# Optimization experiments

Measured on AMD Instinct MI355X. Metric: run time of the kernel, lower is better.

## Reference

```python
import jax, jax.numpy as jnp
import numpy as np

B, N, F, H = 8, 256, 512, 256  # batch, nodes (=hidden_dim), feature_dim, hidden_dim


def _pair_scores(x, y, W1a, W1b, b1, W2, b2):
    """sigmoid(MLP(concat(x_i, y_j))) for all pairs, without materializing concat.

    x, y: [B, N, H]. W1a/W1b are the two halves of the Linear(2H -> H) weight.
    Returns [B, N, N].
    """
    a = jnp.einsum('bnh,hk->bnk', x, W1a)          # contribution of row i
    c = jnp.einsum('bnh,hk->bnk', y, W1b)          # contribution of row j
    h = jax.nn.relu(a[:, :, None, :] + c[:, None, :, :] + b1)  # [B,N,N,H]
    s = jnp.einsum('bijh,h->bij', h, W2) + b2
    return jax.nn.sigmoid(s)


def setup_inputs() -> dict:
    key = jax.random.key(0)
    ks = jax.random.split(key, 16)
    sc = 0.02
    return {
        'image_features': jax.random.normal(ks[0], (B, N, F), jnp.float32),
        'text_features': jax.random.normal(ks[1], (B, N, F), jnp.float32),
        # feature_transform: Linear(F->H), ReLU, Linear(H->H)
        'ft_W1': jax.random.normal(ks[2], (F, H), jnp.float32) * sc,
        'ft_b1': jnp.zeros((H,), jnp.float32),
        'ft_W2': jax.random.normal(ks[3], (H, H), jnp.float32) * sc,
        'ft_b2': jnp.zeros((H,), jnp.float32),
        # structure_learning: Linear(2H->H) split into two H x H halves, Linear(H->1)
        'sl_W1a': jax.random.normal(ks[4], (H, H), jnp.float32) * sc,
        'sl_W1b': jax.random.normal(ks[5], (H, H), jnp.float32) * sc,
        'sl_b1': jnp.zeros((H,), jnp.float32),
        'sl_W2': jax.random.normal(ks[6], (H,), jnp.float32) * sc,
        'sl_b2': jnp.zeros((), jnp.float32),
        # causal_net: Linear(2H->H) split, Linear(H->1)
        'cn_W1a': jax.random.normal(ks[7], (H, H), jnp.float32) * sc,
        'cn_W1b': jax.random.normal(ks[8], (H, H), jnp.float32) * sc,
        'cn_b1': jnp.zeros((H,), jnp.float32),
        'cn_W2': jax.random.normal(ks[9], (H,), jnp.float32) * sc,
        'cn_b2': jnp.zeros((), jnp.float32),
    }


def reference(image_features, text_features,
              ft_W1, ft_b1, ft_W2, ft_b2,
              sl_W1a, sl_W1b, sl_b1, sl_W2, sl_b2,
              cn_W1a, cn_W1b, cn_b1, cn_W2, cn_b2):
    # --- StructuralLearning ---
    def feat(x):
        h = jax.nn.relu(jnp.einsum('bnf,fh->bnh', x, ft_W1) + ft_b1)
        return jnp.einsum('bnh,hk->bnk', h, ft_W2) + ft_b2

    img_h = feat(image_features)   # [B,N,H]
    txt_h = feat(text_features)    # [B,N,H]
    structure = _pair_scores(img_h, txt_h, sl_W1a, sl_W1b, sl_b1, sl_W2, sl_b2)  # [B,N,N]

    # --- CausalDiscovery (batched over all node pairs; sigmoid(structure) > 0
    # everywhere so every (i,j) is an edge). DAG cycle removal is a CPU-side
    # networkx post-process and is omitted from the differentiable reference. ---
    causal_matrix = _pair_scores(structure, structure, cn_W1a, cn_W1b, cn_b1, cn_W2, cn_b2)

    # --- verify_causal_invariance ---
    stability = jnp.mean(jnp.abs(causal_matrix - jnp.roll(causal_matrix, 1, axis=0)))
    consistency = jnp.mean(jnp.std(causal_matrix, axis=0, ddof=1))  # torch.std is unbiased
    invariance_score = 1.0 - (stability + consistency) / 2

    return structure, causal_matrix, invariance_score
```

## Files before the change

### kernel.cpp

```cpp
#include <hip/hip_runtime.h>
#include <math.h>

#define B_ 8
#define N_ 256
#define F_ 512
#define H_ 256

typedef __attribute__((ext_vector_type(8))) short short8;
typedef __attribute__((ext_vector_type(4))) float floatx4;

__device__ __forceinline__ unsigned int f2bf_bits(float f) {
    unsigned int u = __float_as_uint(f);
    return (u + 0x7fffu + ((u >> 16) & 1u)) >> 16;
}
__device__ __forceinline__ unsigned int pack2bf(float a, float b) {
    return f2bf_bits(a) | (f2bf_bits(b) << 16);
}

__global__ __launch_bounds__(256) void prep_weights(
    const float* __restrict__ ftW1, const float* __restrict__ ftW2,
    const float* __restrict__ slW1a, const float* __restrict__ slW1b,
    const float* __restrict__ cnW1a, const float* __restrict__ cnW1b,
    const float* __restrict__ ftb2, const float* __restrict__ slb1,
    unsigned short* __restrict__ wt, float* __restrict__ bA, float* __restrict__ bB)
{
    if (blockIdx.x >= 224) {
        const int second = (blockIdx.x == 225);
        const float* W = second ? slW1b : slW1a;
        const int n = threadIdx.x;
        float s0 = 0.f, s1 = 0.f, s2 = 0.f, s3 = 0.f;
#pragma unroll 4
        for (int k = 0; k < 256; k += 4) {
            s0 = fmaf(ftb2[k],     W[(k)     * 256 + n], s0);
            s1 = fmaf(ftb2[k + 1], W[(k + 1) * 256 + n], s1);
            s2 = fmaf(ftb2[k + 2], W[(k + 2) * 256 + n], s2);
            s3 = fmaf(ftb2[k + 3], W[(k + 3) * 256 + n], s3);
        }
        float s = (s0 + s1) + (s2 + s3);
        if (second) bB[n] = s + slb1[n];
        else        bA[n] = s;
        return;
    }

    int t = blockIdx.x * 256 + threadIdx.x;
    if (t < 49152) {
        const float* src; int K; unsigned short* dst;
        if (t < 16384) { src = ftW1; K = 512; dst = wt; }
        else {
            int m  = (t - 16384) >> 13;
            t = (t - 16384) & 8191; K = 256;
            switch (m) {
                case 0:  src = slW1a; dst = wt + 131072; break;
                case 1:  src = slW1b; dst = wt + 196608; break;
                case 2:  src = cnW1a; dst = wt + 262144; break;
                default: src = cnW1b; dst = wt + 327680; break;
            }
        }
        const int n  = t & 255;
        const int k0 = (t >> 8) * 8;
        unsigned int p[4];
#pragma unroll
        for (int j = 0; j < 4; ++j) {
            float f0 = src[(size_t)(k0 + 2 * j)     * 256 + n];
            float f1 = src[(size_t)(k0 + 2 * j + 1) * 256 + n];
            p[j] = pack2bf(f0, f1);
        }
        *(uint4*)(dst + (size_t)n * K + k0) = make_uint4(p[0], p[1], p[2], p[3]);
    } else {
        const int lt = t - 49152;
        const int k  = lt >> 5;
        const int n0 = (lt & 31) * 8;
        const float* src = ftW2 + (size_t)k * 256 + n0;
        float4 f0 = *(const float4*)(src);
        float4 f1 = *(const float4*)(src + 4);
        unsigned short* dst = wt + 393216 + (size_t)k * 256 + n0;
        *(uint4*)dst = make_uint4(pack2bf(f0.x, f0.y), pack2bf(f0.z, f0.w),
                                  pack2bf(f1.x, f1.y), pack2bf(f1.z, f1.w));
    }
}

__global__ __launch_bounds__(256) void gemm_mfma(
    const void* __restrict__ A0, const void* __restrict__ A1, int aSplitBlk, int aBf16,
    const unsigned short* __restrict__ Wt0, const unsigned short* __restrict__ Wt1,
    const float* __restrict__ bias0, const float* __restrict__ bias1,
    int wRowSplitBlk, int wColSplitBlk,
    void* __restrict__ out, int outBf16, int ldOut, int K, int relu)
{
    __shared__ unsigned short As[2][64][40];
    __shared__ unsigned short Bs[2][64][40];

    const int tid = threadIdx.x;
    const int bx = blockIdx.x, by = blockIdx.y;

    const void* Abase; int arow0;
    if (by < aSplitBlk) { Abase = A0; arow0 = by * 64; }
    else                { Abase = A1; arow0 = (by - aSplitBlk) * 64; }

    int wcolBlk = bx;
    bool second;
    if (wColSplitBlk > 0) {
        second = (bx >= wColSplitBlk);
        if (second) wcolBlk = bx - wColSplitBlk;
    } else {
        second = (by >= wRowSplitBlk);
    }
    const unsigned short* Wt = second ? Wt1 : Wt0;
    const float* bias        = second ? bias1 : bias0;
    const int wcol = wcolBlk * 64;

    const int r    = tid >> 2;
    const int kq   = (tid & 3) * 8;
    const int lane = tid & 63;
    const int wv   = tid >> 6;
    const int col  = lane & 15;
    const int quad = lane >> 4;

    floatx4 acc[4] = {};

    uint4 apack, bpack;
    float4 af0, af1;
    const unsigned short* Abf = (const unsigned short*)Abase + (size_t)(arow0 + r) * K + kq;
    const float*          Afp = (const float*)Abase + (size_t)(arow0 + r) * K + kq;
    const unsigned short* Wp  = Wt + (size_t)(wcol + r) * K + kq;

    if (aBf16) apack = *(const uint4*)(Abf);
    else { af0 = *(const float4*)(Afp); af1 = *(const float4*)(Afp + 4); }
    bpack = *(const uint4*)(Wp);

    int p = 0;
    for (int k0 = 0; k0 < K; k0 += 32) {
        uint4 aw;
        if (aBf16) aw = apack;
        else aw = make_uint4(pack2bf(af0.x, af0.y), pack2bf(af0.z, af0.w),
                             pack2bf(af1.x, af1.y), pack2bf(af1.z, af1.w));
        uint4 bw = bpack;

        *(uint4*)&As[p][r][kq] = aw;
        *(uint4*)&Bs[p][r][kq] = bw;

        if (k0 + 32 < K) {
            if (aBf16) apack = *(const uint4*)(Abf + k0 + 32);
            else {
                af0 = *(const float4*)(Afp + k0 + 32);
                af1 = *(const float4*)(Afp + k0 + 32 + 4);
            }
            bpack = *(const uint4*)(Wp + k0 + 32);
        }

        __syncthreads();

        short8 bfrag = *(const short8*)&Bs[p][wv * 16 + col][quad * 8];
#pragma unroll
        for (int tm = 0; tm < 4; ++tm) {
            short8 afrag = *(const short8*)&As[p][tm * 16 + col][quad * 8];
            acc[tm] = __builtin_amdgcn_mfma_f32_16x16x32_bf16(afrag, bfrag, acc[tm], 0, 0, 0);
        }
        p ^= 1;
    }

    const int ocol = bx * 64 + wv * 16 + col;
    const int bcol = wcol + wv * 16 + col;
    const float bv = bias ? bias[bcol] : 0.f;
#pragma unroll
    for (int tm = 0; tm < 4; ++tm) {
#pragma unroll
        for (int rr = 0; rr < 4; ++rr) {
            float v = acc[tm][rr] + bv;
            if (relu) v = fmaxf(v, 0.f);
            const size_t o = (size_t)(by * 64 + tm * 16 + quad * 4 + rr) * ldOut + ocol;
            if (outBf16) ((unsigned short*)out)[o] = (unsigned short)f2bf_bits(v);
            else         ((float*)out)[o] = v;
        }
    }
}

__global__ __launch_bounds__(256) void pair_score(
    const float* __restrict__ Abase, int ldA,
    const float* __restrict__ Cbase, int ldC,
    const float* __restrict__ W2, const float* __restrict__ b2p,
    float* __restrict__ out)
{
    __shared__ float aS[32][256];
    __shared__ float cS[32][256];

    const int tid = threadIdx.x;
    const int b   = blockIdx.z;
    const int i0b = blockIdx.y * 32;
    const int j0b = blockIdx.x * 32;

    {
        const int r   = tid >> 3;
        const int c8  = tid & 7;
        const int key = (r >> 1) & 7;
        const float* Ar = Abase + ((size_t)b * N_ + i0b + r) * ldA;
        const float* Cr = Cbase + ((size_t)b * N_ + j0b + r) * ldC;
#pragma unroll
        for (int rep = 0; rep < 8; ++rep) {
            const int ch = c8 + rep * 8;
            float4 va = *(const float4*)(Ar + ch * 4);
            float4 vc = *(const float4*)(Cr + ch * 4);
            const int pc = (ch ^ key) << 2;
            *(float4*)&aS[r][pc] = va;
            *(float4*)&cS[r][pc] = vc;
        }
    }
    __syncthreads();

    const int ti = tid >> 4, tj = tid & 15;
    const int ia = ti * 2, jc = tj * 2;
    const int keyA = ti & 7, keyC = tj & 7;

    float s00 = 0.f, s01 = 0.f, s10 = 0.f, s11 = 0.f;
#pragma unroll 4
    for (int h = 0; h < H_; h += 4) {
        const int chunk = h >> 2;
        const int pa = (chunk ^ keyA) << 2;
        const int pc = (chunk ^ keyC) << 2;
        float4 a0 = *(const float4*)&aS[ia][pa];
        float4 a1 = *(const float4*)&aS[ia + 1][pa];
        float4 c0 = *(const float4*)&cS[jc][pc];
        float4 c1 = *(const float4*)&cS[jc + 1][pc];
        float4 w  = *(const float4*)&W2[h];
        float av0[4] = { a0.x, a0.y, a0.z, a0.w };
        float av1[4] = { a1.x, a1.y, a1.z, a1.w };
        float cv0[4] = { c0.x, c0.y, c0.z, c0.w };
        float cv1[4] = { c1.x, c1.y, c1.z, c1.w };
        float wv[4]  = { w.x,  w.y,  w.z,  w.w  };
#pragma unroll
        for (int q = 0; q < 4; ++q) {
            s00 = fmaf(fmaxf(av0[q] + cv0[q], 0.f), wv[q], s00);
            s01 = fmaf(fmaxf(av0[q] + cv1[q], 0.f), wv[q], s01);
            s10 = fmaf(fmaxf(av1[q] + cv0[q], 0.f), wv[q], s10);
            s11 = fmaf(fmaxf(av1[q] + cv1[q], 0.f), wv[q], s11);
        }
    }
    const float bb = b2p[0];
    const size_t ob = ((size_t)b * N_ + i0b + ia) * N_ + j0b + jc;
    out[ob]           = 1.f / (1.f + expf(-(s00 + bb)));
    out[ob + 1]       = 1.f / (1.f + expf(-(s01 + bb)));
    out[ob + N_]      = 1.f / (1.f + expf(-(s10 + bb)));
    out[ob + N_ + 1]  = 1.f / (1.f + expf(-(s11 + bb)));
}

__global__ __launch_bounds__(256) void invariance_partial(
    const float* __restrict__ causal, float* __restrict__ accum,
    float* __restrict__ out_scalar)
{
    const int idx = blockIdx.x * 256 + threadIdx.x;
    float x[B_];
#pragma unroll
    for (int b = 0; b < B_; ++b) x[b] = causal[(size_t)b * (N_ * N_) + idx];

    float stab = 0.f, mean = 0.f;
#pragma unroll
    for (int b = 0; b < B_; ++b) {
        stab += fabsf(x[b] - x[(b + B_ - 1) % B_]);
        mean += x[b];
    }
    mean *= (1.f / B_);
    float var = 0.f;
#pragma unroll
    for (int b = 0; b < B_; ++b) {
        float d = x[b] - mean;
        var = fmaf(d, d, var);
    }
    float sd = sqrtf(var * (1.f / (B_ - 1)));

#pragma unroll
    for (int off = 32; off > 0; off >>= 1) {
        stab += __shfl_down(stab, off, 64);
        sd   += __shfl_down(sd, off, 64);
    }

    __shared__ float red[8];
    if ((threadIdx.x & 63) == 0) {
        red[threadIdx.x >> 6]     = stab;
        red[4 + (threadIdx.x >> 6)] = sd;
    }
    __syncthreads();
    if (threadIdx.x == 0) {
        float s = (red[0] + red[1]) + (red[2] + red[3]);
        float d = (red[4] + red[5]) + (red[6] + red[7]);
        atomicAdd(&accum[0], s);
        atomicAdd(&accum[1], d);
        __threadfence();
        unsigned int prev = atomicAdd((unsigned int*)&accum[2], 1u);
        if (prev == 255u) {
            float st  = atomicAdd(&accum[0], 0.f);
            float sdt = atomicAdd(&accum[1], 0.f);
            float stability   = st  * (1.f / (float)(B_ * N_ * N_));
            float consistency = sdt * (1.f / (float)(N_ * N_));
            out_scalar[0] = 1.f - (stability + consistency) * 0.5f;
        }
    }
}

extern "C" void kernel_launch(void* const* d_in, const int* in_sizes, int n_in,
                              void* d_out, int out_size, void* d_ws, size_t ws_size,
                              hipStream_t stream)
{
    const float* img   = (const float*)d_in[0];
    const float* txt   = (const float*)d_in[1];
    const float* ftW1  = (const float*)d_in[2];
    const float* ftb1  = (const float*)d_in[3];
    const float* ftW2  = (const float*)d_in[4];
    const float* ftb2  = (const float*)d_in[5];
    const float* slW1a = (const float*)d_in[6];
    const float* slW1b = (const float*)d_in[7];
    const float* slb1  = (const float*)d_in[8];
    const float* slW2  = (const float*)d_in[9];
    const float* slb2  = (const float*)d_in[10];
    const float* cnW1a = (const float*)d_in[11];
    const float* cnW1b = (const float*)d_in[12];
    const float* cnb1  = (const float*)d_in[13];
    const float* cnW2  = (const float*)d_in[14];
    const float* cnb2  = (const float*)d_in[15];

    float* out       = (float*)d_out;
    float* structure = out;
    float* causal    = out + (size_t)B_ * N_ * N_;
    float* inv       = out + 2 * (size_t)B_ * N_ * N_;

    unsigned short* wt     = (unsigned short*)d_ws;
    unsigned short* wcombT = wt + 458752;
    float* bA    = (float*)(wt + 589824);
    float* bB    = bA + 256;
    float* accum = bA + 512;
    unsigned short* h1b = wt + 655360;
    float* acb   = (float*)(wt + 1703936);
    float* ac2b  = acb;

    hipMemsetAsync(accum, 0, 4 * sizeof(float), stream);

    dim3 blk(256);
    const int BIG = 1 << 20;

    const unsigned short* wtFT1 = wt;
    const unsigned short* wtSLA = wt + 131072;
    const unsigned short* wtSLB = wt + 196608;
    const unsigned short* wtCNA = wt + 262144;
    const unsigned short* wtCNB = wt + 327680;
    const unsigned short* ftW2r = wt + 393216;

    prep_weights<<<dim3(226), blk, 0, stream>>>(
        ftW1, ftW2, slW1a, slW1b, cnW1a, cnW1b, ftb2, slb1, wt, bA, bB);

    gemm_mfma<<<dim3(4, 8), blk, 0, stream>>>(
        wtSLA, wtSLB, 4, 1, ftW2r, ftW2r, nullptr, nullptr, BIG, 0,
        wcombT, 1, 256, 256, 0);

    gemm_mfma<<<dim3(4, 64), blk, 0, stream>>>(
        img, txt, 32, 0, wtFT1, wtFT1, ftb1, ftb1, BIG, 0,
        h1b, 1, 256, 512, 1);

    gemm_mfma<<<dim3(4, 64), blk, 0, stream>>>(
        h1b, h1b, BIG, 1, wcombT, wcombT + 65536, bA, bB, 32, 0,
        acb, 0, 256, 256, 0);

    pair_score<<<dim3(8, 8, 8), blk, 0, stream>>>(
        acb, 256, acb + (size_t)2048 * 256, 256, slW2, slb2, structure);

    gemm_mfma<<<dim3(8, 32), blk, 0, stream>>>(
        structure, structure, BIG, 0, wtCNA, wtCNB, nullptr, cnb1, BIG, 4,
        ac2b, 0, 512, 256, 0);

    pair_score<<<dim3(8, 8, 8), blk, 0, stream>>>(
        ac2b, 512, ac2b + 256, 512, cnW2, cnb2, causal);

    invariance_partial<<<dim3(N_ * N_ / 256), blk, 0, stream>>>(causal, accum, inv);
}
```

Measured before the change: 176.9 us.

## Use packed fp16 pair-score math, larger tiles, and merge two GEMM launches

The pair-score intermediates are now written by the GEMMs as fp16 instead of fp32. The pair-score kernel does the add and ReLU with packed half2 arithmetic and accumulates in fp32. Its tile grows to 64x32 with 4x2 outputs per thread, which halves LDS footprint per row and raises reuse. The first feature GEMM and the weight-combining GEMM are merged into one launch through a job struct, saving a launch and letting them overlap. The cost is reduced precision in the pre-ReLU sums, which adds accuracy risk.

```diff
diff --git a/kernel.cpp b/kernel.cpp
--- a/kernel.cpp
+++ b/kernel.cpp
@@ -8,6 +8,7 @@
 
 typedef __attribute__((ext_vector_type(8))) short short8;
 typedef __attribute__((ext_vector_type(4))) float floatx4;
+typedef _Float16 h2 __attribute__((ext_vector_type(2)));
 
 __device__ __forceinline__ unsigned int f2bf_bits(float f) {
     unsigned int u = __float_as_uint(f);
@@ -15,6 +16,19 @@
 }
 __device__ __forceinline__ unsigned int pack2bf(float a, float b) {
     return f2bf_bits(a) | (f2bf_bits(b) << 16);
+}
+__device__ __forceinline__ h2 as_h2(unsigned int u) {
+    union { unsigned int u; h2 h; } x; x.u = u; return x.h;
+}
+__device__ __forceinline__ h2 relu2(h2 t) {
+    h2 z; z.x = (_Float16)0; z.y = (_Float16)0;
+#if __has_builtin(__builtin_elementwise_max)
+    return __builtin_elementwise_max(t, z);
+#else
+    t.x = t.x > z.x ? t.x : z.x;
+    t.y = t.y > z.y ? t.y : z.y;
+    return t;
+#endif
 }
 
 __global__ __launch_bounds__(256) void prep_weights(
@@ -79,33 +93,40 @@
     }
 }
 
-__global__ __launch_bounds__(256) void gemm_mfma(
-    const void* __restrict__ A0, const void* __restrict__ A1, int aSplitBlk, int aBf16,
-    const unsigned short* __restrict__ Wt0, const unsigned short* __restrict__ Wt1,
-    const float* __restrict__ bias0, const float* __restrict__ bias1,
-    int wRowSplitBlk, int wColSplitBlk,
-    void* __restrict__ out, int outBf16, int ldOut, int K, int relu)
+struct GJob {
+    const void* A0; const void* A1; int aSplitBlk; int aBf16;
+    const unsigned short* Wt0; const unsigned short* Wt1;
+    const float* bias0; const float* bias1;
+    int wRowSplitBlk; int wColSplitBlk;
+    void* out; int outMode; int ldOut; int K; int relu;
+};
+
+__global__ __launch_bounds__(256) void gemm_mfma(GJob j0, GJob j1, int j0By)
 {
     __shared__ unsigned short As[2][64][40];
     __shared__ unsigned short Bs[2][64][40];
 
+    const bool firstJob = ((int)blockIdx.y < j0By);
+    const GJob j = firstJob ? j0 : j1;
+    const int by = firstJob ? blockIdx.y : blockIdx.y - j0By;
+    const int bx = blockIdx.x;
     const int tid = threadIdx.x;
-    const int bx = blockIdx.x, by = blockIdx.y;
+    const int K = j.K;
 
     const void* Abase; int arow0;
-    if (by < aSplitBlk) { Abase = A0; arow0 = by * 64; }
-    else                { Abase = A1; arow0 = (by - aSplitBlk) * 64; }
+    if (by < j.aSplitBlk) { Abase = j.A0; arow0 = by * 64; }
+    else                  { Abase = j.A1; arow0 = (by - j.aSplitBlk) * 64; }
 
     int wcolBlk = bx;
     bool second;
-    if (wColSplitBlk > 0) {
-        second = (bx >= wColSplitBlk);
-        if (second) wcolBlk = bx - wColSplitBlk;
+    if (j.wColSplitBlk > 0) {
+        second = (bx >= j.wColSplitBlk);
+        if (second) wcolBlk = bx - j.wColSplitBlk;
     } else {
-        second = (by >= wRowSplitBlk);
-    }
-    const unsigned short* Wt = second ? Wt1 : Wt0;
-    const float* bias        = second ? bias1 : bias0;
+        second = (by >= j.wRowSplitBlk);
+    }
+    const unsigned short* Wt = second ? j.Wt1 : j.Wt0;
+    const float* bias        = second ? j.bias1 : j.bias0;
     const int wcol = wcolBlk * 64;
 
     const int r    = tid >> 2;
@@ -123,14 +144,14 @@
     const float*          Afp = (const float*)Abase + (size_t)(arow0 + r) * K + kq;
     const unsigned short* Wp  = Wt + (size_t)(wcol + r) * K + kq;
 
-    if (aBf16) apack = *(const uint4*)(Abf);
+    if (j.aBf16) apack = *(const uint4*)(Abf);
     else { af0 = *(const float4*)(Afp); af1 = *(const float4*)(Afp + 4); }
     bpack = *(const uint4*)(Wp);
 
     int p = 0;
     for (int k0 = 0; k0 < K; k0 += 32) {
         uint4 aw;
-        if (aBf16) aw = apack;
+        if (j.aBf16) aw = apack;
         else aw = make_uint4(pack2bf(af0.x, af0.y), pack2bf(af0.z, af0.w),
                              pack2bf(af1.x, af1.y), pack2bf(af1.z, af1.w));
         uint4 bw = bpack;
@@ -139,7 +160,7 @@
         *(uint4*)&Bs[p][r][kq] = bw;
 
         if (k0 + 32 < K) {
-            if (aBf16) apack = *(const uint4*)(Abf + k0 + 32);
+            if (j.aBf16) apack = *(const uint4*)(Abf + k0 + 32);
             else {
                 af0 = *(const float4*)(Afp + k0 + 32);
                 af1 = *(const float4*)(Afp + k0 + 32 + 4);
@@ -166,80 +187,100 @@
 #pragma unroll
         for (int rr = 0; rr < 4; ++rr) {
             float v = acc[tm][rr] + bv;
-            if (relu) v = fmaxf(v, 0.f);
-            const size_t o = (size_t)(by * 64 + tm * 16 + quad * 4 + rr) * ldOut + ocol;
-            if (outBf16) ((unsigned short*)out)[o] = (unsigned short)f2bf_bits(v);
-            else         ((float*)out)[o] = v;
+            if (j.relu) v = fmaxf(v, 0.f);
+            const size_t o = (size_t)(by * 64 + tm * 16 + quad * 4 + rr) * j.ldOut + ocol;
+            if (j.outMode == 0)      ((float*)j.out)[o] = v;
+            else if (j.outMode == 1) ((unsigned short*)j.out)[o] = (unsigned short)f2bf_bits(v);
+            else                     ((_Float16*)j.out)[o] = (_Float16)v;
         }
     }
 }
 
 __global__ __launch_bounds__(256) void pair_score(
-    const float* __restrict__ Abase, int ldA,
-    const float* __restrict__ Cbase, int ldC,
+    const unsigned short* __restrict__ Abase, int ldA,
+    const unsigned short* __restrict__ Cbase, int ldC,
     const float* __restrict__ W2, const float* __restrict__ b2p,
     float* __restrict__ out)
 {
-    __shared__ float aS[32][256];
-    __shared__ float cS[32][256];
+    __shared__ unsigned short aS[64][256];
+    __shared__ unsigned short cS[32][256];
 
     const int tid = threadIdx.x;
     const int b   = blockIdx.z;
-    const int i0b = blockIdx.y * 32;
+    const int i0b = blockIdx.y * 64;
     const int j0b = blockIdx.x * 32;
 
     {
-        const int r   = tid >> 3;
-        const int c8  = tid & 7;
-        const int key = (r >> 1) & 7;
-        const float* Ar = Abase + ((size_t)b * N_ + i0b + r) * ldA;
-        const float* Cr = Cbase + ((size_t)b * N_ + j0b + r) * ldC;
+        const int rr = tid >> 3;
+        const int c8 = tid & 7;
 #pragma unroll
         for (int rep = 0; rep < 8; ++rep) {
-            const int ch = c8 + rep * 8;
-            float4 va = *(const float4*)(Ar + ch * 4);
-            float4 vc = *(const float4*)(Cr + ch * 4);
-            const int pc = (ch ^ key) << 2;
-            *(float4*)&aS[r][pc] = va;
-            *(float4*)&cS[r][pc] = vc;
+            const int li = rr + 32 * (rep & 1);
+            const int ch = c8 + 8 * (rep >> 1);
+            uint4 v = *(const uint4*)(Abase + ((size_t)b * N_ + i0b + li) * ldA + ch * 8);
+            *(uint4*)&aS[li][(ch ^ ((li >> 1) & 7)) * 8] = v;
+        }
+#pragma unroll
+        for (int rep = 0; rep < 4; ++rep) {
+            const int ch = c8 + 8 * rep;
+            uint4 v = *(const uint4*)(Cbase + ((size_t)b * N_ + j0b + rr) * ldC + ch * 8);
+            *(uint4*)&cS[rr][(ch ^ ((rr >> 1) & 7)) * 8] = v;
         }
     }
     __syncthreads();
 
     const int ti = tid >> 4, tj = tid & 15;
-    const int ia = ti * 2, jc = tj * 2;
-    const int keyA = ti & 7, keyC = tj & 7;
-
-    float s00 = 0.f, s01 = 0.f, s10 = 0.f, s11 = 0.f;
+    const int ia = ti * 4, jc = tj * 2;
+    const int k01 = (2 * ti) & 7;
+    const int k23 = (2 * ti + 1) & 7;
+    const int kc  = tj & 7;
+
+    float s[4][2] = {};
+
 #pragma unroll 4
-    for (int h = 0; h < H_; h += 4) {
-        const int chunk = h >> 2;
-        const int pa = (chunk ^ keyA) << 2;
-        const int pc = (chunk ^ keyC) << 2;
-        float4 a0 = *(const float4*)&aS[ia][pa];
-        float4 a1 = *(const float4*)&aS[ia + 1][pa];
-        float4 c0 = *(const float4*)&cS[jc][pc];
-        float4 c1 = *(const float4*)&cS[jc + 1][pc];
-        float4 w  = *(const float4*)&W2[h];
-        float av0[4] = { a0.x, a0.y, a0.z, a0.w };
-        float av1[4] = { a1.x, a1.y, a1.z, a1.w };
-        float cv0[4] = { c0.x, c0.y, c0.z, c0.w };
-        float cv1[4] = { c1.x, c1.y, c1.z, c1.w };
-        float wv[4]  = { w.x,  w.y,  w.z,  w.w  };
-#pragma unroll
-        for (int q = 0; q < 4; ++q) {
-            s00 = fmaf(fmaxf(av0[q] + cv0[q], 0.f), wv[q], s00);
-            s01 = fmaf(fmaxf(av0[q] + cv1[q], 0.f), wv[q], s01);
-            s10 = fmaf(fmaxf(av1[q] + cv0[q], 0.f), wv[q], s10);
-            s11 = fmaf(fmaxf(av1[q] + cv1[q], 0.f), wv[q], s11);
-        }
-    }
+    for (int ch = 0; ch < 32; ++ch) {
+        const uint4 a0 = *(const uint4*)&aS[ia    ][(ch ^ k01) * 8];
+        const uint4 a1 = *(const uint4*)&aS[ia + 1][(ch ^ k01) * 8];
+        const uint4 a2 = *(const uint4*)&aS[ia + 2][(ch ^ k23) * 8];
+        const uint4 a3 = *(const uint4*)&aS[ia + 3][(ch ^ k23) * 8];
+        const uint4 c0 = *(const uint4*)&cS[jc    ][(ch ^ kc) * 8];
+        const uint4 c1 = *(const uint4*)&cS[jc + 1][(ch ^ kc) * 8];
+        const float* w = &W2[ch * 8];
+#pragma unroll
+        for (int u = 0; u < 4; ++u) {
+            const float w0 = w[2 * u], w1 = w[2 * u + 1];
+            const h2 hc0 = as_h2(((const unsigned int*)&c0)[u]);
+            const h2 hc1 = as_h2(((const unsigned int*)&c1)[u]);
+#define ACC2(su, ha, hc) { h2 t_ = relu2((ha) + (hc)); \
+    su = fmaf((float)t_.x, w0, su); su = fmaf((float)t_.y, w1, su); }
+            {
+                const h2 ha = as_h2(((const unsigned int*)&a0)[u]);
+                ACC2(s[0][0], ha, hc0); ACC2(s[0][1], ha, hc1);
+            }
+            {
+                const h2 ha = as_h2(((const unsigned int*)&a1)[u]);
+                ACC2(s[1][0], ha, hc0); ACC2(s[1][1], ha, hc1);
+            }
+            {
+                const h2 ha = as_h2(((const unsigned int*)&a2)[u]);
+                ACC2(s[2][0], ha, hc0); ACC2(s[2][1], ha, hc1);
+            }
+            {
+                const h2 ha = as_h2(((const unsigned int*)&a3)[u]);
+                ACC2(s[3][0], ha, hc0); ACC2(s[3][1], ha, hc1);
+            }
+#undef ACC2
+        }
+    }
+
     const float bb = b2p[0];
-    const size_t ob = ((size_t)b * N_ + i0b + ia) * N_ + j0b + jc;
-    out[ob]           = 1.f / (1.f + expf(-(s00 + bb)));
-    out[ob + 1]       = 1.f / (1.f + expf(-(s01 + bb)));
-    out[ob + N_]      = 1.f / (1.f + expf(-(s10 + bb)));
-    out[ob + N_ + 1]  = 1.f / (1.f + expf(-(s11 + bb)));
+#pragma unroll
+    for (int rr = 0; rr < 4; ++rr) {
+        float2 o;
+        o.x = 1.f / (1.f + expf(-(s[rr][0] + bb)));
+        o.y = 1.f / (1.f + expf(-(s[rr][1] + bb)));
+        *(float2*)&out[((size_t)b * N_ + i0b + ia + rr) * N_ + j0b + jc] = o;
+    }
 }
 
 __global__ __launch_bounds__(256) void invariance_partial(
@@ -274,7 +315,7 @@
 
     __shared__ float red[8];
     if ((threadIdx.x & 63) == 0) {
-        red[threadIdx.x >> 6]     = stab;
+        red[threadIdx.x >> 6]       = stab;
         red[4 + (threadIdx.x >> 6)] = sd;
     }
     __syncthreads();
@@ -326,9 +367,9 @@
     float* bA    = (float*)(wt + 589824);
     float* bB    = bA + 256;
     float* accum = bA + 512;
-    unsigned short* h1b = wt + 655360;
-    float* acb   = (float*)(wt + 1703936);
-    float* ac2b  = acb;
+    unsigned short* h1b  = wt + 655360;
+    unsigned short* acb  = wt + 1703936;
+    unsigned short* ac2b = acb;
 
     hipMemsetAsync(accum, 0, 4 * sizeof(float), stream);
 
@@ -345,26 +386,30 @@
     prep_weights<<<dim3(226), blk, 0, stream>>>(
         ftW1, ftW2, slW1a, slW1b, cnW1a, cnW1b, ftb2, slb1, wt, bA, bB);
 
-    gemm_mfma<<<dim3(4, 8), blk, 0, stream>>>(
-        wtSLA, wtSLB, 4, 1, ftW2r, ftW2r, nullptr, nullptr, BIG, 0,
-        wcombT, 1, 256, 256, 0);
-
-    gemm_mfma<<<dim3(4, 64), blk, 0, stream>>>(
-        img, txt, 32, 0, wtFT1, wtFT1, ftb1, ftb1, BIG, 0,
-        h1b, 1, 256, 512, 1);
-
-    gemm_mfma<<<dim3(4, 64), blk, 0, stream>>>(
-        h1b, h1b, BIG, 1, wcombT, wcombT + 65536, bA, bB, 32, 0,
-        acb, 0, 256, 256, 0);
-
-    pair_score<<<dim3(8, 8, 8), blk, 0, stream>>>(
+    {
+        GJob g1  = { img, txt, 32, 0, wtFT1, wtFT1, ftb1, ftb1, BIG, 0,
+                     h1b, 1, 256, 512, 1 };
+        GJob wcb = { wtSLA, wtSLB, 4, 1, ftW2r, ftW2r, nullptr, nullptr, BIG, 0,
+                     wcombT, 1, 256, 256, 0 };
+        gemm_mfma<<<dim3(4, 72), blk, 0, stream>>>(g1, wcb, 64);
+    }
+
+    {
+        GJob g2 = { h1b, h1b, BIG, 1, wcombT, wcombT + 65536, bA, bB, 32, 0,
+                    acb, 2, 256, 256, 0 };
+        gemm_mfma<<<dim3(4, 64), blk, 0, stream>>>(g2, g2, 64);
+    }
+
+    pair_score<<<dim3(8, 4, 8), blk, 0, stream>>>(
         acb, 256, acb + (size_t)2048 * 256, 256, slW2, slb2, structure);
 
-    gemm_mfma<<<dim3(8, 32), blk, 0, stream>>>(
-        structure, structure, BIG, 0, wtCNA, wtCNB, nullptr, cnb1, BIG, 4,
-        ac2b, 0, 512, 256, 0);
-
-    pair_score<<<dim3(8, 8, 8), blk, 0, stream>>>(
+    {
+        GJob g4 = { structure, structure, BIG, 0, wtCNA, wtCNB, nullptr, cnb1, BIG, 4,
+                    ac2b, 2, 512, 256, 0 };
+        gemm_mfma<<<dim3(8, 32), blk, 0, stream>>>(g4, g4, 32);
+    }
+
+    pair_score<<<dim3(8, 4, 8), blk, 0, stream>>>(
         ac2b, 512, ac2b + 256, 512, cnW2, cnb2, causal);
 
     invariance_partial<<<dim3(N_ * N_ / 256), blk, 0, stream>>>(causal, accum, inv);
```

Result: faster. 166.8 us (-5.7%).
